# Performance work log

Hardware: AMD Instinct MI355X
Metric: run time of the kernel (lower is better)

Reference implementation:

```python
import jax, jax.numpy as jnp
import numpy as np

NMIX = 10  # mixtures in discretized mix of logistics


def _causal_mask(kh, kw, include_center):
    # rows strictly above center fully visible; center row left of center; optionally center
    m = np.zeros((kh, kw), dtype=np.float32)
    m[: kh // 2, :] = 1.0
    m[kh // 2, : kw // 2] = 1.0
    if include_center:
        m[kh // 2, kw // 2] = 1.0
    return jnp.asarray(m)[None, None]  # [1,1,kh,kw] broadcast over O,I


def _conv(x, w):
    return jax.lax.conv_general_dilated(
        x, w, (1, 1), 'SAME', dimension_numbers=('NCHW', 'OIHW', 'NCHW'))


def pixelcnn_params(x, w_in, w_blk, w_out1, w_out2):
    mA = _causal_mask(7, 7, False)
    mB = _causal_mask(3, 3, True)
    h = _conv(x, w_in * mA)                      # [B,160,H,W]
    for i in range(w_blk.shape[0]):              # 5 gated resnet blocks
        g = _conv(jax.nn.relu(h), w_blk[i] * mB)  # [B,320,H,W]
        a, b = jnp.split(g, 2, axis=1)
        h = h + jnp.tanh(a) * jax.nn.sigmoid(b)
    h = jax.nn.relu(_conv(jax.nn.relu(h), w_out1))
    return _conv(h, w_out2)                      # [B,100,H,W]


def dmol_log_prob(x, params):
    # x: [B,3,H,W] in [-1,1]; params: [B,100,H,W]; returns per-example log prob [B]
    B, C, H, W = x.shape
    l = jnp.transpose(params, (0, 2, 3, 1))       # [B,H,W,100]
    xt = jnp.transpose(x, (0, 2, 3, 1))           # [B,H,W,3]
    logit_probs = l[..., :NMIX]                   # [B,H,W,10]
    rest = l[..., NMIX:].reshape(B, H, W, 3, 3 * NMIX)
    means = rest[..., :NMIX]
    log_scales = jnp.maximum(rest[..., NMIX:2 * NMIX], -7.0)
    coeffs = jnp.tanh(rest[..., 2 * NMIX:])
    xe = xt[..., None]                            # [B,H,W,3,1]
    m1 = means[..., 0, :]
    m2 = means[..., 1, :] + coeffs[..., 0, :] * xe[..., 0, :]
    m3 = means[..., 2, :] + coeffs[..., 1, :] * xe[..., 0, :] + coeffs[..., 2, :] * xe[..., 1, :]
    means_adj = jnp.stack([m1, m2, m3], axis=3)   # [B,H,W,3,10]
    centered = xe - means_adj
    inv_stdv = jnp.exp(-log_scales)
    plus_in = inv_stdv * (centered + 1.0 / 255.0)
    min_in = inv_stdv * (centered - 1.0 / 255.0)
    cdf_delta = jax.nn.sigmoid(plus_in) - jax.nn.sigmoid(min_in)
    log_cdf_plus = plus_in - jax.nn.softplus(plus_in)
    log_one_minus_cdf_min = -jax.nn.softplus(min_in)
    mid_in = inv_stdv * centered
    log_pdf_mid = mid_in - log_scales - 2.0 * jax.nn.softplus(mid_in)
    log_prob_in = jnp.where(cdf_delta > 1e-5,
                            jnp.log(jnp.clip(cdf_delta, 1e-12, None)),
                            log_pdf_mid - np.float32(np.log(127.5)))
    log_probs_c = jnp.where(xe < -0.999, log_cdf_plus,
                            jnp.where(xe > 0.999, log_one_minus_cdf_min, log_prob_in))
    log_probs = jnp.sum(log_probs_c, axis=3) + jax.nn.log_softmax(logit_probs, axis=-1)
    lp = jax.scipy.special.logsumexp(log_probs, axis=-1)  # [B,H,W]
    return jnp.sum(lp, axis=(1, 2))                       # [B]


def setup_inputs() -> dict:
    key = jax.random.key(0)
    ks = jax.random.split(key, 5)
    F = 160
    return {
        'samples': jax.random.uniform(ks[0], (16, 3, 64, 64), dtype=jnp.float32),
        'w_in': jax.random.normal(ks[1], (F, 3, 7, 7), dtype=jnp.float32) * 0.05,
        'w_blk': jax.random.normal(ks[2], (5, 2 * F, F, 3, 3), dtype=jnp.float32) * 0.03,
        'w_out1': jax.random.normal(ks[3], (F, F, 1, 1), dtype=jnp.float32) * 0.05,
        'w_out2': jax.random.normal(ks[4], (100, F, 1, 1), dtype=jnp.float32) * 0.05,
    }


def reference(samples, w_in, w_blk, w_out1, w_out2):
    x = samples * 2.0 - 1.0
    params = pixelcnn_params(x, w_in, w_blk, w_out1, w_out2)
    return dmol_log_prob(x, params)
```

## Files before the change

kernel.cpp:

```cpp
#include <hip/hip_runtime.h>
#include <math.h>


using short8  = __attribute__((ext_vector_type(8))) short;
using short4v = __attribute__((ext_vector_type(4))) short;
using f32x4   = __attribute__((ext_vector_type(4))) float;

static constexpr float L2E = 1.44269504088896f;
static constexpr float LN2 = 0.69314718055995f;

__device__ __forceinline__ float fexp2(float x) { return __builtin_amdgcn_exp2f(x); }
__device__ __forceinline__ float flog2(float x) { return __builtin_amdgcn_logf(x); }
__device__ __forceinline__ float frcp(float x)  { return __builtin_amdgcn_rcpf(x); }
__device__ __forceinline__ float fexp(float x)  { return fexp2(x * L2E); }
__device__ __forceinline__ float flog(float x)  { return flog2(x) * LN2; }
__device__ __forceinline__ float fsigmoid(float x) { return frcp(1.f + fexp2(-x * L2E)); }
__device__ __forceinline__ float ftanh(float x)    { return 1.f - 2.f * frcp(1.f + fexp2(x * (2.f * L2E))); }
__device__ __forceinline__ float fsoftplus(float z) {
    float e = fexp2(-fabsf(z) * L2E);
    return fmaxf(z, 0.f) + flog2(1.f + e) * LN2;
}

__device__ __forceinline__ unsigned pk_bf16(float a, float b) {
    union { float f; unsigned u; } ua, ub; ua.f = a; ub.f = b;
    return __builtin_amdgcn_perm(ub.u + 0x7fffu, ua.u + 0x7fffu, 0x07060302u);
}

__device__ __forceinline__ short f2bf(float f) {
    union { float f; unsigned u; } v; v.f = f;
    unsigned r = (v.u + 0x7fffu + ((v.u >> 16) & 1u)) >> 16;
    return (short)r;
}

__device__ __forceinline__ short8 pack8_relu(float4 a, float4 b) {
    union { short8 s; unsigned u[4]; } r;
    r.u[0] = pk_bf16(fmaxf(a.x, 0.f), fmaxf(a.y, 0.f));
    r.u[1] = pk_bf16(fmaxf(a.z, 0.f), fmaxf(a.w, 0.f));
    r.u[2] = pk_bf16(fmaxf(b.x, 0.f), fmaxf(b.y, 0.f));
    r.u[3] = pk_bf16(fmaxf(b.z, 0.f), fmaxf(b.w, 0.f));
    return r.s;
}

static constexpr size_t X_OFF    = 0;
static constexpr size_t WINP_OFF = 786432;
static constexpr size_t W1P_OFF  = 817152;
static constexpr size_t W2P_OFF  = 868352;
static constexpr size_t WPB_OFF  = 919552;
static constexpr size_t HA_OFF   = 3479552;
static constexpr size_t HB_OFF   = 45422592;

__global__ void k_prep(const float* __restrict__ s, float* __restrict__ x, int n) {
    int i = blockIdx.x * 256 + threadIdx.x;
    if (i < n) x[i] = 2.f * s[i] - 1.f;
}

__global__ void k_twb(const float* __restrict__ w, short* __restrict__ wP) {
    int idx = blockIdx.x * 256 + threadIdx.x;
    if (idx >= 5 * 25 * 320 * 32) return;
    int icl = idx & 31;
    int oc  = (idx >> 5) % 320;
    int kt  = ((idx >> 5) / 320) % 25;
    int i   = idx / (25 * 320 * 32);
    int tap = kt / 5, ic = (kt % 5) * 32 + icl;
    const int ky[5] = {0,0,0,1,1}, kx[5] = {0,1,2,0,1};
    float v = w[(((size_t)(i * 320 + oc) * 160 + ic) * 3 + ky[tap]) * 3 + kx[tap]];
    wP[idx] = f2bf(v);
}

__global__ void k_twin(const float* __restrict__ w, short* __restrict__ wP) {
    int idx = blockIdx.x * 256 + threadIdx.x;
    if (idx >= 3 * 160 * 32) return;
    int icl = idx & 31;
    int oc  = (idx >> 5) % 160;
    int kc  = idx / 5120;
    int k = kc * 32 + icl;
    short v = 0;
    if (k < 72) {
        int tap = k / 3, ic = k % 3;
        int ky = (tap < 21) ? tap / 7 : 3;
        int kx = (tap < 21) ? tap % 7 : tap - 21;
        v = f2bf(w[((oc * 3 + ic) * 7 + ky) * 7 + kx]);
    }
    wP[idx] = v;
}

__global__ void k_tw1(const float* __restrict__ w, short* __restrict__ wP) {
    int idx = blockIdx.x * 256 + threadIdx.x;
    if (idx >= 5 * 160 * 32) return;
    int icl = idx & 31;
    int oc  = (idx >> 5) % 160;
    int kc  = idx / 5120;
    wP[idx] = f2bf(w[oc * 160 + kc * 32 + icl]);
}

__global__ void k_tw2(const float* __restrict__ w, short* __restrict__ wP) {
    int idx = blockIdx.x * 256 + threadIdx.x;
    if (idx >= 5 * 160 * 32) return;
    int icl = idx & 31;
    int oc  = (idx >> 5) % 160;
    int kc  = idx / 5120;
    wP[idx] = (oc < 100) ? f2bf(w[oc * 160 + kc * 32 + icl]) : (short)0;
}

__global__ __launch_bounds__(320) void k_convin(const float* __restrict__ X,
                                                const short* __restrict__ WINP,
                                                float* __restrict__ hout) {
    __shared__ float xls[3 * 4 * 72];
    __shared__ short Bls[64 * 104];
    int y = blockIdx.x, b = blockIdx.y;
    int t = threadIdx.x;
    for (int i = t; i < 840; i += 320) {
        int col = i % 70; int r = (i / 70) % 4; int ic = i / 280;
        int xg = col - 3, yg = y + r - 3;
        float v = 0.f;
        if (xg >= 0 && xg < 64 && yg >= 0)
            v = X[((size_t)(b * 3 + ic) * 64 + yg) * 64 + xg];
        xls[(ic * 4 + r) * 72 + col] = v;
    }
    __syncthreads();
    for (int i = t; i < 6144; i += 320) {
        int k = i % 96; int px = i / 96;
        short v = 0;
        if (k < 72) {
            int tap = k / 3, ic = k % 3;
            int ky = (tap < 21) ? tap / 7 : 3;
            int kx = (tap < 21) ? tap % 7 : tap - 21;
            v = f2bf(xls[(ic * 4 + ky) * 72 + px + kx]);
        }
        Bls[px * 104 + k] = v;
    }
    __syncthreads();
    int lane = t & 63, w = t >> 6;
    int lx = lane & 15, q = lane >> 4;
    f32x4 acc[2][4] = {};
    const short* wl = WINP + lx * 32 + q * 8;
    #pragma unroll
    for (int kc = 0; kc < 3; ++kc) {
        short8 aF[2], bF[4];
        aF[0] = *(const short8*)(wl + (kc * 160 + 32 * w) * 32);
        aF[1] = *(const short8*)(wl + (kc * 160 + 32 * w + 16) * 32);
        #pragma unroll
        for (int nt = 0; nt < 4; ++nt)
            bF[nt] = *(const short8*)&Bls[(nt * 16 + lx) * 104 + kc * 32 + q * 8];
        #pragma unroll
        for (int mt = 0; mt < 2; ++mt)
            #pragma unroll
            for (int nt = 0; nt < 4; ++nt)
                acc[mt][nt] = __builtin_amdgcn_mfma_f32_16x16x32_bf16(
                    aF[mt], bF[nt], acc[mt][nt], 0, 0, 0);
    }
    size_t rowbase = ((size_t)(b * 64 + y)) * 64 * 160;
    #pragma unroll
    for (int mt = 0; mt < 2; ++mt) {
        int c0 = 32 * w + mt * 16 + q * 4;
        #pragma unroll
        for (int nt = 0; nt < 4; ++nt) {
            int px = nt * 16 + lx;
            float4 o;
            o.x = acc[mt][nt][0]; o.y = acc[mt][nt][1];
            o.z = acc[mt][nt][2]; o.w = acc[mt][nt][3];
            *(float4*)&hout[rowbase + (size_t)px * 160 + c0] = o;
        }
    }
}

__global__ __launch_bounds__(320, 4) void k_blk(const float* __restrict__ hin,
                                                float* __restrict__ hout,
                                                const short* __restrict__ wP) {
    __shared__ short in_s[2 * 66 * 168];
    int y = blockIdx.x, b = blockIdx.y;
    int t = threadIdx.x;
    for (int i = t; i < 2640; i += 320) {
        int c8 = i % 20; int xl = (i / 20) % 66; int r = i / 1320;
        int xg = xl - 1, yg = y + r - 1;
        short8 v = {};
        if (xg >= 0 && xg < 64 && yg >= 0) {
            const float* p = hin + (((size_t)(b * 64 + yg)) * 64 + xg) * 160 + c8 * 8;
            v = pack8_relu(*(const float4*)p, *(const float4*)(p + 4));
        }
        *(short8*)&in_s[(r * 66 + xl) * 168 + c8 * 8] = v;
    }
    __syncthreads();

    int lane = t & 63, w = t >> 6;
    int lx = lane & 15, q = lane >> 4;
    f32x4 acc[4][4] = {};
    const short* wl = wP + lx * 32 + q * 8;
    const int dxs[5] = {-1, 0, 1, -1, 0};
    const int rws[5] = {0, 0, 0, 1, 1};
    #pragma unroll
    for (int tap = 0; tap < 5; ++tap) {
        int rb0 = (rws[tap] * 66 + 1 + dxs[tap] + lx) * 168 + q * 8;
        #pragma unroll
        for (int k5 = 0; k5 < 5; ++k5) {
            const short* wk = wl + (tap * 5 + k5) * 10240;
            short8 aF[4], bF[4];
            aF[0] = *(const short8*)(wk + (32 * w) * 32);
            aF[1] = *(const short8*)(wk + (32 * w + 16) * 32);
            aF[2] = *(const short8*)(wk + (160 + 32 * w) * 32);
            aF[3] = *(const short8*)(wk + (176 + 32 * w) * 32);
            int rb = rb0 + k5 * 32;
            #pragma unroll
            for (int nt = 0; nt < 4; ++nt)
                bF[nt] = *(const short8*)&in_s[rb + nt * 16 * 168];
            #pragma unroll
            for (int mt = 0; mt < 4; ++mt)
                #pragma unroll
                for (int nt = 0; nt < 4; ++nt)
                    acc[mt][nt] = __builtin_amdgcn_mfma_f32_16x16x32_bf16(
                        aF[mt], bF[nt], acc[mt][nt], 0, 0, 0);
        }
    }
    size_t rowbase = ((size_t)(b * 64 + y)) * 64 * 160;
    #pragma unroll
    for (int mt = 0; mt < 2; ++mt) {
        int c0 = 32 * w + mt * 16 + q * 4;
        #pragma unroll
        for (int nt = 0; nt < 4; ++nt) {
            int px = nt * 16 + lx;
            size_t off = rowbase + (size_t)px * 160 + c0;
            float4 ho = *(const float4*)&hin[off];
            float4 o;
            o.x = ho.x + ftanh(acc[mt][nt][0]) * fsigmoid(acc[mt + 2][nt][0]);
            o.y = ho.y + ftanh(acc[mt][nt][1]) * fsigmoid(acc[mt + 2][nt][1]);
            o.z = ho.z + ftanh(acc[mt][nt][2]) * fsigmoid(acc[mt + 2][nt][2]);
            o.w = ho.w + ftanh(acc[mt][nt][3]) * fsigmoid(acc[mt + 2][nt][3]);
            *(float4*)&hout[off] = o;
        }
    }
}

__global__ __launch_bounds__(320) void k_head(const float* __restrict__ hin,
                                              const short* __restrict__ W1P,
                                              const short* __restrict__ W2P,
                                              const float* __restrict__ X,
                                              float* __restrict__ out) {
    __shared__ char arenaA[29696];
    __shared__ short h2ls[64 * 168];
    short* hls = (short*)arenaA;
    float* Pls = (float*)arenaA;
    float* lpls = (float*)(arenaA + 26624);
    int y = blockIdx.x, b = blockIdx.y;
    int t = threadIdx.x;
    size_t rowbase = ((size_t)(b * 64 + y)) * 64 * 160;
    for (int i = t; i < 1280; i += 320) {
        int c8 = i % 20; int px = i / 20;
        const float* p = hin + rowbase + (size_t)px * 160 + c8 * 8;
        *(short8*)&hls[px * 168 + c8 * 8] = pack8_relu(*(const float4*)p, *(const float4*)(p + 4));
    }
    __syncthreads();
    int lane = t & 63, w = t >> 6;
    int lx = lane & 15, q = lane >> 4;
    {
        f32x4 acc[2][4] = {};
        const short* wl = W1P + lx * 32 + q * 8;
        #pragma unroll
        for (int kc = 0; kc < 5; ++kc) {
            short8 aF[2], bF[4];
            aF[0] = *(const short8*)(wl + (kc * 160 + 32 * w) * 32);
            aF[1] = *(const short8*)(wl + (kc * 160 + 32 * w + 16) * 32);
            #pragma unroll
            for (int nt = 0; nt < 4; ++nt)
                bF[nt] = *(const short8*)&hls[(nt * 16 + lx) * 168 + kc * 32 + q * 8];
            #pragma unroll
            for (int mt = 0; mt < 2; ++mt)
                #pragma unroll
                for (int nt = 0; nt < 4; ++nt)
                    acc[mt][nt] = __builtin_amdgcn_mfma_f32_16x16x32_bf16(
                        aF[mt], bF[nt], acc[mt][nt], 0, 0, 0);
        }
        #pragma unroll
        for (int mt = 0; mt < 2; ++mt) {
            int c0 = 32 * w + mt * 16 + q * 4;
            #pragma unroll
            for (int nt = 0; nt < 4; ++nt) {
                int px = nt * 16 + lx;
                union { short4v s; unsigned u[2]; } sv;
                sv.u[0] = pk_bf16(fmaxf(acc[mt][nt][0], 0.f), fmaxf(acc[mt][nt][1], 0.f));
                sv.u[1] = pk_bf16(fmaxf(acc[mt][nt][2], 0.f), fmaxf(acc[mt][nt][3], 0.f));
                *(short4v*)&h2ls[px * 168 + c0] = sv.s;
            }
        }
    }
    __syncthreads();
    {
        f32x4 acc[2][4] = {};
        const short* wl = W2P + lx * 32 + q * 8;
        #pragma unroll
        for (int kc = 0; kc < 5; ++kc) {
            short8 aF[2], bF[4];
            aF[0] = *(const short8*)(wl + (kc * 160 + 32 * w) * 32);
            aF[1] = *(const short8*)(wl + (kc * 160 + 32 * w + 16) * 32);
            #pragma unroll
            for (int nt = 0; nt < 4; ++nt)
                bF[nt] = *(const short8*)&h2ls[(nt * 16 + lx) * 168 + kc * 32 + q * 8];
            #pragma unroll
            for (int mt = 0; mt < 2; ++mt)
                #pragma unroll
                for (int nt = 0; nt < 4; ++nt)
                    acc[mt][nt] = __builtin_amdgcn_mfma_f32_16x16x32_bf16(
                        aF[mt], bF[nt], acc[mt][nt], 0, 0, 0);
        }
        #pragma unroll
        for (int mt = 0; mt < 2; ++mt) {
            int c0 = 32 * w + mt * 16 + q * 4;
            if (c0 < 100) {
                #pragma unroll
                for (int nt = 0; nt < 4; ++nt) {
                    int px = nt * 16 + lx;
                    float4 o;
                    o.x = acc[mt][nt][0]; o.y = acc[mt][nt][1];
                    o.z = acc[mt][nt][2]; o.w = acc[mt][nt][3];
                    *(float4*)&Pls[px * 104 + c0] = o;
                }
            }
        }
    }
    __syncthreads();
    const float LOG127P5 = 4.8481163504f;
    #pragma unroll
    for (int it = 0; it < 2; ++it) {
        int tk = t + it * 320;
        int px = tk & 63, m = tk >> 6;
        const float* pp = &Pls[px * 104];
        float xs[3];
        #pragma unroll
        for (int c = 0; c < 3; ++c)
            xs[c] = X[((size_t)(b * 3 + c)) * 4096 + (size_t)y * 64 + px];
        float mx = pp[0];
        #pragma unroll
        for (int j = 1; j < 10; ++j) mx = fmaxf(mx, pp[j]);
        float se = 0.f;
        #pragma unroll
        for (int j = 0; j < 10; ++j) se += fexp(pp[j] - mx);
        float lse = mx + flog(se);
        float sum = pp[m] - lse;
        float mean0 = pp[10 + m];
        float mean1 = pp[40 + m];
        float mean2 = pp[70 + m];
        float ls0 = fmaxf(pp[20 + m], -7.f);
        float ls1 = fmaxf(pp[50 + m], -7.f);
        float ls2 = fmaxf(pp[80 + m], -7.f);
        float c0 = ftanh(pp[30 + m]);
        float c1 = ftanh(pp[60 + m]);
        float c2 = ftanh(pp[90 + m]);
        float mu[3], lsv[3];
        mu[0] = mean0;
        mu[1] = mean1 + c0 * xs[0];
        mu[2] = mean2 + c1 * xs[0] + c2 * xs[1];
        lsv[0] = ls0; lsv[1] = ls1; lsv[2] = ls2;
        #pragma unroll
        for (int ci = 0; ci < 3; ++ci) {
            float cent = xs[ci] - mu[ci];
            float inv = fexp(-lsv[ci]);
            float plus_in = inv * (cent + 1.f / 255.f);
            float min_in = inv * (cent - 1.f / 255.f);
            float cdf_delta = fsigmoid(plus_in) - fsigmoid(min_in);
            float log_cdf_plus = plus_in - fsoftplus(plus_in);
            float log_om_cdf = -fsoftplus(min_in);
            float mid = inv * cent;
            float log_pdf_mid = mid - lsv[ci] - 2.f * fsoftplus(mid);
            float lpi = (cdf_delta > 1e-5f) ? flog(fmaxf(cdf_delta, 1e-12f))
                                            : (log_pdf_mid - LOG127P5);
            float lpc = (xs[ci] < -0.999f) ? log_cdf_plus
                       : ((xs[ci] > 0.999f) ? log_om_cdf : lpi);
            sum += lpc;
        }
        lpls[px * 12 + m] = sum;
    }
    __syncthreads();
    if (t < 64) {
        int px = t;
        float mx2 = lpls[px * 12];
        #pragma unroll
        for (int m = 1; m < 10; ++m) mx2 = fmaxf(mx2, lpls[px * 12 + m]);
        float se2 = 0.f;
        #pragma unroll
        for (int m = 0; m < 10; ++m) se2 += fexp(lpls[px * 12 + m] - mx2);
        float lp = mx2 + flog(se2);
        #pragma unroll
        for (int off = 32; off > 0; off >>= 1) lp += __shfl_down(lp, off, 64);
        if (t == 0) atomicAdd(&out[b], lp);
    }
}

extern "C" void kernel_launch(void* const* d_in, const int* in_sizes, int n_in,
                              void* d_out, int out_size, void* d_ws, size_t ws_size,
                              hipStream_t stream) {
    const float* samples = (const float*)d_in[0];
    const float* w_in    = (const float*)d_in[1];
    const float* w_blk   = (const float*)d_in[2];
    const float* w_out1  = (const float*)d_in[3];
    const float* w_out2  = (const float*)d_in[4];
    char* ws = (char*)d_ws;
    float* X    = (float*)(ws + X_OFF);
    short* WINP = (short*)(ws + WINP_OFF);
    short* W1P  = (short*)(ws + W1P_OFF);
    short* W2P  = (short*)(ws + W2P_OFF);
    short* WPB  = (short*)(ws + WPB_OFF);
    float* HA   = (float*)(ws + HA_OFF);
    float* HB   = (float*)(ws + HB_OFF);
    float* fout = (float*)d_out;

    k_prep<<<768, 256, 0, stream>>>(samples, X, 16 * 3 * 4096);
    k_twb<<<5000, 256, 0, stream>>>(w_blk, WPB);
    k_twin<<<60, 256, 0, stream>>>(w_in, WINP);
    k_tw1<<<100, 256, 0, stream>>>(w_out1, W1P);
    k_tw2<<<100, 256, 0, stream>>>(w_out2, W2P);

    k_convin<<<dim3(64, 16), 320, 0, stream>>>(X, WINP, HA);

    float* a = HA; float* bq = HB;
    for (int i = 0; i < 5; i++) {
        k_blk<<<dim3(64, 16), 320, 0, stream>>>(a, bq, WPB + (size_t)i * 25 * 320 * 32);
        float* tmp = a; a = bq; bq = tmp;
    }
    hipMemsetAsync(d_out, 0, (size_t)out_size * sizeof(float), stream);
    k_head<<<dim3(64, 16), 320, 0, stream>>>(a, W1P, W2P, X, fout);
}
```

Before: 448.2 us.

## Store residual activations in bf16 and split each row across two blocks

The residual stream h between layers is now stored as bf16 instead of fp32. This halves global traffic for every block's load and store, and ReLU is applied with a bitmask on the packed values. Each image row is also split into two 32-pixel halves, doubling the grid and reducing shared memory and accumulators per block, which allows more occupancy and parallelism. The cost is accumulated rounding error in the residual path across five blocks, plus more halo reloads per block.

Result: slower. 540.0 us (+20.5%).

```diff
diff --git a/kernel.cpp b/kernel.cpp
--- a/kernel.cpp
+++ b/kernel.cpp
@@ -32,13 +32,13 @@
     return (short)r;
 }
 
-__device__ __forceinline__ short8 pack8_relu(float4 a, float4 b) {
-    union { short8 s; unsigned u[4]; } r;
-    r.u[0] = pk_bf16(fmaxf(a.x, 0.f), fmaxf(a.y, 0.f));
-    r.u[1] = pk_bf16(fmaxf(a.z, 0.f), fmaxf(a.w, 0.f));
-    r.u[2] = pk_bf16(fmaxf(b.x, 0.f), fmaxf(b.y, 0.f));
-    r.u[3] = pk_bf16(fmaxf(b.z, 0.f), fmaxf(b.w, 0.f));
-    return r.s;
+__device__ __forceinline__ float bf2f(unsigned short s) {
+    union { unsigned u; float f; } v; v.u = ((unsigned)s) << 16; return v.f;
+}
+
+__device__ __forceinline__ unsigned relu2(unsigned v) {
+    unsigned m = ((v & 0x80008000u) >> 15) * 0xffffu;
+    return v & ~m;
 }
 
 static constexpr size_t X_OFF    = 0;
@@ -47,7 +47,7 @@
 static constexpr size_t W2P_OFF  = 868352;
 static constexpr size_t WPB_OFF  = 919552;
 static constexpr size_t HA_OFF   = 3479552;
-static constexpr size_t HB_OFF   = 45422592;
+static constexpr size_t HB_OFF   = 24451072;
 
 __global__ void k_prep(const float* __restrict__ s, float* __restrict__ x, int n) {
     int i = blockIdx.x * 256 + threadIdx.x;
@@ -104,48 +104,49 @@
 
 __global__ __launch_bounds__(320) void k_convin(const float* __restrict__ X,
                                                 const short* __restrict__ WINP,
-                                                float* __restrict__ hout) {
-    __shared__ float xls[3 * 4 * 72];
-    __shared__ short Bls[64 * 104];
-    int y = blockIdx.x, b = blockIdx.y;
+                                                unsigned short* __restrict__ hout) {
+    __shared__ float xls[3 * 4 * 40];
+    __shared__ short Bls[32 * 104];
+    int y = blockIdx.x >> 1, half = blockIdx.x & 1, b = blockIdx.y;
+    int xbase = half * 32;
     int t = threadIdx.x;
-    for (int i = t; i < 840; i += 320) {
-        int col = i % 70; int r = (i / 70) % 4; int ic = i / 280;
-        int xg = col - 3, yg = y + r - 3;
+    for (int i = t; i < 456; i += 320) {
+        int col = i % 38; int r = (i / 38) % 4; int ic = i / 152;
+        int xg = xbase + col - 3, yg = y + r - 3;
         float v = 0.f;
         if (xg >= 0 && xg < 64 && yg >= 0)
             v = X[((size_t)(b * 3 + ic) * 64 + yg) * 64 + xg];
-        xls[(ic * 4 + r) * 72 + col] = v;
-    }
-    __syncthreads();
-    for (int i = t; i < 6144; i += 320) {
+        xls[(ic * 4 + r) * 40 + col] = v;
+    }
+    __syncthreads();
+    for (int i = t; i < 3072; i += 320) {
         int k = i % 96; int px = i / 96;
         short v = 0;
         if (k < 72) {
             int tap = k / 3, ic = k % 3;
             int ky = (tap < 21) ? tap / 7 : 3;
             int kx = (tap < 21) ? tap % 7 : tap - 21;
-            v = f2bf(xls[(ic * 4 + ky) * 72 + px + kx]);
+            v = f2bf(xls[(ic * 4 + ky) * 40 + px + kx]);
         }
         Bls[px * 104 + k] = v;
     }
     __syncthreads();
     int lane = t & 63, w = t >> 6;
     int lx = lane & 15, q = lane >> 4;
-    f32x4 acc[2][4] = {};
+    f32x4 acc[2][2] = {};
     const short* wl = WINP + lx * 32 + q * 8;
     #pragma unroll
     for (int kc = 0; kc < 3; ++kc) {
-        short8 aF[2], bF[4];
+        short8 aF[2], bF[2];
         aF[0] = *(const short8*)(wl + (kc * 160 + 32 * w) * 32);
         aF[1] = *(const short8*)(wl + (kc * 160 + 32 * w + 16) * 32);
         #pragma unroll
-        for (int nt = 0; nt < 4; ++nt)
+        for (int nt = 0; nt < 2; ++nt)
             bF[nt] = *(const short8*)&Bls[(nt * 16 + lx) * 104 + kc * 32 + q * 8];
         #pragma unroll
         for (int mt = 0; mt < 2; ++mt)
             #pragma unroll
-            for (int nt = 0; nt < 4; ++nt)
+            for (int nt = 0; nt < 2; ++nt)
                 acc[mt][nt] = __builtin_amdgcn_mfma_f32_16x16x32_bf16(
                     aF[mt], bF[nt], acc[mt][nt], 0, 0, 0);
     }
@@ -154,59 +155,59 @@
     for (int mt = 0; mt < 2; ++mt) {
         int c0 = 32 * w + mt * 16 + q * 4;
         #pragma unroll
-        for (int nt = 0; nt < 4; ++nt) {
-            int px = nt * 16 + lx;
-            float4 o;
-            o.x = acc[mt][nt][0]; o.y = acc[mt][nt][1];
-            o.z = acc[mt][nt][2]; o.w = acc[mt][nt][3];
-            *(float4*)&hout[rowbase + (size_t)px * 160 + c0] = o;
-        }
-    }
-}
-
-__global__ __launch_bounds__(320, 4) void k_blk(const float* __restrict__ hin,
-                                                float* __restrict__ hout,
-                                                const short* __restrict__ wP) {
-    __shared__ short in_s[2 * 66 * 168];
-    int y = blockIdx.x, b = blockIdx.y;
+        for (int nt = 0; nt < 2; ++nt) {
+            int px = xbase + nt * 16 + lx;
+            uint2 o;
+            o.x = pk_bf16(acc[mt][nt][0], acc[mt][nt][1]);
+            o.y = pk_bf16(acc[mt][nt][2], acc[mt][nt][3]);
+            *(uint2*)&hout[rowbase + (size_t)px * 160 + c0] = o;
+        }
+    }
+}
+
+__global__ __launch_bounds__(320) void k_blk(const unsigned short* __restrict__ hin,
+                                             unsigned short* __restrict__ hout,
+                                             const short* __restrict__ wP) {
+    __shared__ short in_s[2 * 34 * 168];
+    int y = blockIdx.x >> 1, half = blockIdx.x & 1, b = blockIdx.y;
+    int xbase = half * 32;
     int t = threadIdx.x;
-    for (int i = t; i < 2640; i += 320) {
-        int c8 = i % 20; int xl = (i / 20) % 66; int r = i / 1320;
-        int xg = xl - 1, yg = y + r - 1;
-        short8 v = {};
+    for (int i = t; i < 1360; i += 320) {
+        int c8 = i % 20; int xl = (i / 20) % 34; int r = i / 680;
+        int xg = xbase + xl - 1, yg = y + r - 1;
+        uint4 v = {0u, 0u, 0u, 0u};
         if (xg >= 0 && xg < 64 && yg >= 0) {
-            const float* p = hin + (((size_t)(b * 64 + yg)) * 64 + xg) * 160 + c8 * 8;
-            v = pack8_relu(*(const float4*)p, *(const float4*)(p + 4));
-        }
-        *(short8*)&in_s[(r * 66 + xl) * 168 + c8 * 8] = v;
+            v = *(const uint4*)&hin[(((size_t)(b * 64 + yg)) * 64 + xg) * 160 + c8 * 8];
+            v.x = relu2(v.x); v.y = relu2(v.y); v.z = relu2(v.z); v.w = relu2(v.w);
+        }
+        *(uint4*)&in_s[(r * 34 + xl) * 168 + c8 * 8] = v;
     }
     __syncthreads();
 
     int lane = t & 63, w = t >> 6;
     int lx = lane & 15, q = lane >> 4;
-    f32x4 acc[4][4] = {};
+    f32x4 acc[4][2] = {};
     const short* wl = wP + lx * 32 + q * 8;
     const int dxs[5] = {-1, 0, 1, -1, 0};
     const int rws[5] = {0, 0, 0, 1, 1};
     #pragma unroll
     for (int tap = 0; tap < 5; ++tap) {
-        int rb0 = (rws[tap] * 66 + 1 + dxs[tap] + lx) * 168 + q * 8;
+        int rb0 = (rws[tap] * 34 + 1 + dxs[tap] + lx) * 168 + q * 8;
         #pragma unroll
         for (int k5 = 0; k5 < 5; ++k5) {
             const short* wk = wl + (tap * 5 + k5) * 10240;
-            short8 aF[4], bF[4];
+            short8 aF[4], bF[2];
             aF[0] = *(const short8*)(wk + (32 * w) * 32);
             aF[1] = *(const short8*)(wk + (32 * w + 16) * 32);
             aF[2] = *(const short8*)(wk + (160 + 32 * w) * 32);
             aF[3] = *(const short8*)(wk + (176 + 32 * w) * 32);
             int rb = rb0 + k5 * 32;
-            #pragma unroll
-            for (int nt = 0; nt < 4; ++nt)
-                bF[nt] = *(const short8*)&in_s[rb + nt * 16 * 168];
+            bF[0] = *(const short8*)&in_s[rb];
+            bF[1] = *(const short8*)&in_s[rb + 16 * 168];
             #pragma unroll
             for (int mt = 0; mt < 4; ++mt)
                 #pragma unroll
-                for (int nt = 0; nt < 4; ++nt)
+                for (int nt = 0; nt < 2; ++nt)
                     acc[mt][nt] = __builtin_amdgcn_mfma_f32_16x16x32_bf16(
                         aF[mt], bF[nt], acc[mt][nt], 0, 0, 0);
         }
@@ -216,64 +217,69 @@
     for (int mt = 0; mt < 2; ++mt) {
         int c0 = 32 * w + mt * 16 + q * 4;
         #pragma unroll
-        for (int nt = 0; nt < 4; ++nt) {
-            int px = nt * 16 + lx;
+        for (int nt = 0; nt < 2; ++nt) {
+            int px = xbase + nt * 16 + lx;
             size_t off = rowbase + (size_t)px * 160 + c0;
-            float4 ho = *(const float4*)&hin[off];
-            float4 o;
-            o.x = ho.x + ftanh(acc[mt][nt][0]) * fsigmoid(acc[mt + 2][nt][0]);
-            o.y = ho.y + ftanh(acc[mt][nt][1]) * fsigmoid(acc[mt + 2][nt][1]);
-            o.z = ho.z + ftanh(acc[mt][nt][2]) * fsigmoid(acc[mt + 2][nt][2]);
-            o.w = ho.w + ftanh(acc[mt][nt][3]) * fsigmoid(acc[mt + 2][nt][3]);
-            *(float4*)&hout[off] = o;
-        }
-    }
-}
-
-__global__ __launch_bounds__(320) void k_head(const float* __restrict__ hin,
+            ushort4 hv = *(const ushort4*)&hin[off];
+            float o0 = bf2f(hv.x) + ftanh(acc[mt][nt][0]) * fsigmoid(acc[mt + 2][nt][0]);
+            float o1 = bf2f(hv.y) + ftanh(acc[mt][nt][1]) * fsigmoid(acc[mt + 2][nt][1]);
+            float o2 = bf2f(hv.z) + ftanh(acc[mt][nt][2]) * fsigmoid(acc[mt + 2][nt][2]);
+            float o3 = bf2f(hv.w) + ftanh(acc[mt][nt][3]) * fsigmoid(acc[mt + 2][nt][3]);
+            uint2 o;
+            o.x = pk_bf16(o0, o1);
+            o.y = pk_bf16(o2, o3);
+            *(uint2*)&hout[off] = o;
+        }
+    }
+}
+
+__global__ __launch_bounds__(320) void k_head(const unsigned short* __restrict__ hin,
                                               const short* __restrict__ W1P,
                                               const short* __restrict__ W2P,
                                               const float* __restrict__ X,
                                               float* __restrict__ out) {
-    __shared__ char arenaA[29696];
-    __shared__ short h2ls[64 * 168];
-    short* hls = (short*)arenaA;
-    float* Pls = (float*)arenaA;
-    float* lpls = (float*)(arenaA + 26624);
-    int y = blockIdx.x, b = blockIdx.y;
+    __shared__ char arena[14848];
+    __shared__ short h2ls[32 * 168];
+    short* hls = (short*)arena;
+    float* Pls = (float*)arena;
+    float* lpls = (float*)(arena + 13312);
+    int y = blockIdx.x >> 1, half = blockIdx.x & 1, b = blockIdx.y;
+    int xbase = half * 32;
     int t = threadIdx.x;
     size_t rowbase = ((size_t)(b * 64 + y)) * 64 * 160;
-    for (int i = t; i < 1280; i += 320) {
+    for (int i = t; i < 640; i += 320) {
         int c8 = i % 20; int px = i / 20;
-        const float* p = hin + rowbase + (size_t)px * 160 + c8 * 8;
-        *(short8*)&hls[px * 168 + c8 * 8] = pack8_relu(*(const float4*)p, *(const float4*)(p + 4));
+        uint4 v = *(const uint4*)&hin[rowbase + (size_t)(xbase + px) * 160 + c8 * 8];
+        v.x = relu2(v.x); v.y = relu2(v.y); v.z = relu2(v.z); v.w = relu2(v.w);
+        *(uint4*)&hls[px * 168 + c8 * 8] = v;
     }
     __syncthreads();
     int lane = t & 63, w = t >> 6;
     int lx = lane & 15, q = lane >> 4;
     {
-        f32x4 acc[2][4] = {};
+        f32x4 acc[2][2] = {};
         const short* wl = W1P + lx * 32 + q * 8;
         #pragma unroll
         for (int kc = 0; kc < 5; ++kc) {
-            short8 aF[2], bF[4];
+            short8 aF[2], bF[2];
             aF[0] = *(const short8*)(wl + (kc * 160 + 32 * w) * 32);
             aF[1] = *(const short8*)(wl + (kc * 160 + 32 * w + 16) * 32);
             #pragma unroll
-            for (int nt = 0; nt < 4; ++nt)
+            for (int nt = 0; nt < 2; ++nt)
                 bF[nt] = *(const short8*)&hls[(nt * 16 + lx) * 168 + kc * 32 + q * 8];
             #pragma unroll
             for (int mt = 0; mt < 2; ++mt)
                 #pragma unroll
-                for (int nt = 0; nt < 4; ++nt)
+                for (int nt = 0; nt < 2; ++nt)
                     acc[mt][nt] = __builtin_amdgcn_mfma_f32_16x16x32_bf16(
                         aF[mt], bF[nt], acc[mt][nt], 0, 0, 0);
         }
+        __syncthreads();
         #pragma unroll
         for (int mt = 0; mt < 2; ++mt) {
             int c0 = 32 * w + mt * 16 + q * 4;
             #pragma unroll
-            for (int nt = 0; nt < 4; ++nt) {
+            for (int nt = 0; nt < 2; ++nt) {
                 int px = nt * 16 + lx;
                 union { short4v s; unsigned u[2]; } sv;
                 sv.u[0] = pk_bf16(fmaxf(acc[mt][nt][0], 0.f), fmaxf(acc[mt][nt][1], 0.f));
@@ -284,20 +290,20 @@
     }
     __syncthreads();
     {
-        f32x4 acc[2][4] = {};
+        f32x4 acc[2][2] = {};
         const short* wl = W2P + lx * 32 + q * 8;
         #pragma unroll
         for (int kc = 0; kc < 5; ++kc) {
-            short8 aF[2], bF[4];
+            short8 aF[2], bF[2];
             aF[0] = *(const short8*)(wl + (kc * 160 + 32 * w) * 32);
             aF[1] = *(const short8*)(wl + (kc * 160 + 32 * w + 16) * 32);
             #pragma unroll
-            for (int nt = 0; nt < 4; ++nt)
+            for (int nt = 0; nt < 2; ++nt)
                 bF[nt] = *(const short8*)&h2ls[(nt * 16 + lx) * 168 + kc * 32 + q * 8];
             #pragma unroll
             for (int mt = 0; mt < 2; ++mt)
                 #pragma unroll
-                for (int nt = 0; nt < 4; ++nt)
+                for (int nt = 0; nt < 2; ++nt)
                     acc[mt][nt] = __builtin_amdgcn_mfma_f32_16x16x32_bf16(
                         aF[mt], bF[nt], acc[mt][nt], 0, 0, 0);
         }
@@ -306,7 +312,7 @@
             int c0 = 32 * w + mt * 16 + q * 4;
             if (c0 < 100) {
                 #pragma unroll
-                for (int nt = 0; nt < 4; ++nt) {
+                for (int nt = 0; nt < 2; ++nt) {
                     int px = nt * 16 + lx;
                     float4 o;
                     o.x = acc[mt][nt][0]; o.y = acc[mt][nt][1];
@@ -318,15 +324,13 @@
     }
     __syncthreads();
     const float LOG127P5 = 4.8481163504f;
-    #pragma unroll
-    for (int it = 0; it < 2; ++it) {
-        int tk = t + it * 320;
-        int px = tk & 63, m = tk >> 6;
+    {
+        int px = t & 31, m = t >> 5;
         const float* pp = &Pls[px * 104];
         float xs[3];
         #pragma unroll
         for (int c = 0; c < 3; ++c)
-            xs[c] = X[((size_t)(b * 3 + c)) * 4096 + (size_t)y * 64 + px];
+            xs[c] = X[((size_t)(b * 3 + c)) * 4096 + (size_t)y * 64 + xbase + px];
         float mx = pp[0];
         #pragma unroll
         for (int j = 1; j < 10; ++j) mx = fmaxf(mx, pp[j]);
@@ -369,7 +373,7 @@
         lpls[px * 12 + m] = sum;
     }
     __syncthreads();
-    if (t < 64) {
+    if (t < 32) {
         int px = t;
         float mx2 = lpls[px * 12];
         #pragma unroll
@@ -378,8 +382,11 @@
         #pragma unroll
         for (int m = 0; m < 10; ++m) se2 += fexp(lpls[px * 12 + m] - mx2);
         float lp = mx2 + flog(se2);
-        #pragma unroll
-        for (int off = 32; off > 0; off >>= 1) lp += __shfl_down(lp, off, 64);
+        lp += __shfl_down(lp, 16, 32);
+        lp += __shfl_down(lp, 8, 32);
+        lp += __shfl_down(lp, 4, 32);
+        lp += __shfl_down(lp, 2, 32);
+        lp += __shfl_down(lp, 1, 32);
         if (t == 0) atomicAdd(&out[b], lp);
     }
 }
@@ -398,8 +405,8 @@
     short* W1P  = (short*)(ws + W1P_OFF);
     short* W2P  = (short*)(ws + W2P_OFF);
     short* WPB  = (short*)(ws + WPB_OFF);
-    float* HA   = (float*)(ws + HA_OFF);
-    float* HB   = (float*)(ws + HB_OFF);
+    unsigned short* HA = (unsigned short*)(ws + HA_OFF);
+    unsigned short* HB = (unsigned short*)(ws + HB_OFF);
     float* fout = (float*)d_out;
 
     k_prep<<<768, 256, 0, stream>>>(samples, X, 16 * 3 * 4096);
@@ -408,13 +415,13 @@
     k_tw1<<<100, 256, 0, stream>>>(w_out1, W1P);
     k_tw2<<<100, 256, 0, stream>>>(w_out2, W2P);
 
-    k_convin<<<dim3(64, 16), 320, 0, stream>>>(X, WINP, HA);
-
-    float* a = HA; float* bq = HB;
+    k_convin<<<dim3(128, 16), 320, 0, stream>>>(X, WINP, HA);
+
+    unsigned short* a = HA; unsigned short* bq = HB;
     for (int i = 0; i < 5; i++) {
-        k_blk<<<dim3(64, 16), 320, 0, stream>>>(a, bq, WPB + (size_t)i * 25 * 320 * 32);
-        float* tmp = a; a = bq; bq = tmp;
+        k_blk<<<dim3(128, 16), 320, 0, stream>>>(a, bq, WPB + (size_t)i * 25 * 320 * 32);
+        unsigned short* tmp = a; a = bq; bq = tmp;
     }
     hipMemsetAsync(d_out, 0, (size_t)out_size * sizeof(float), stream);
-    k_head<<<dim3(64, 16), 320, 0, stream>>>(a, W1P, W2P, X, fout);
-}
+    k_head<<<dim3(128, 16), 320, 0, stream>>>(a, W1P, W2P, X, fout);
+}
```
